# Performance work log

Hardware: AMD Instinct MI355X
Metric: run time of the kernel (lower is better)

Reference implementation:

```python
import jax, jax.numpy as jnp
import numpy as np

B, T, D_MODEL = 1, 4096, 1024
H = 16
SEM_DIM, GEO_DIM, ATTN_DIM = 128, 256, 512
SEM_HD, GEO_HD, V_HD = SEM_DIM // H, GEO_DIM // H, ATTN_DIM // H
ROPE_BASE = 10000.0


def _split_heads(x, hd):
    # (B,T,H*hd) -> (B,H,T,hd)
    b, t, _ = x.shape
    return x.reshape(b, t, H, hd).transpose(0, 2, 1, 3)


def _rope(x, pos_offset, base=ROPE_BASE):
    # x: (B,H,T,rot) with rot == full geo head dim (rotate applies to first rot_dim;
    # here rot_dim == geo_head_dim so the whole vector rotates)
    rot = x.shape[-1]
    inv_freq = 1.0 / (base ** (jnp.arange(0, rot, 2, dtype=jnp.float32) / rot))
    t = jnp.arange(pos_offset, pos_offset + x.shape[2], dtype=jnp.float32)
    freqs = t[:, None] * inv_freq[None, :]            # (T, rot/2)
    cos = jnp.cos(freqs).astype(x.dtype)[None, None]  # (1,1,T,rot/2)
    sin = jnp.sin(freqs).astype(x.dtype)[None, None]
    x1, x2 = x[..., : rot // 2], x[..., rot // 2 :]
    return jnp.concatenate([x1 * cos - x2 * sin, x1 * sin + x2 * cos], axis=-1)


def setup_inputs() -> dict:
    key = jax.random.key(0)
    ks = jax.random.split(key, 8)
    s = lambda fan_in: 1.0 / np.sqrt(fan_in)
    inp = {
        "x": jax.random.normal(ks[0], (B, T, D_MODEL), dtype=jnp.float32),
        "q_sem_w": jax.random.uniform(ks[1], (SEM_DIM, D_MODEL), jnp.float32, -s(D_MODEL), s(D_MODEL)),
        "k_sem_w": jax.random.uniform(ks[2], (SEM_DIM, D_MODEL), jnp.float32, -s(D_MODEL), s(D_MODEL)),
        "q_geo_w": jax.random.uniform(ks[3], (GEO_DIM, D_MODEL), jnp.float32, -s(D_MODEL), s(D_MODEL)),
        "k_geo_w": jax.random.uniform(ks[4], (GEO_DIM, D_MODEL), jnp.float32, -s(D_MODEL), s(D_MODEL)),
        "v_w": jax.random.uniform(ks[5], (ATTN_DIM, D_MODEL), jnp.float32, -s(D_MODEL), s(D_MODEL)),
        "out_w": jax.random.uniform(ks[6], (D_MODEL, ATTN_DIM), jnp.float32, -s(ATTN_DIM), s(ATTN_DIM)),
        "logit_scale": jnp.zeros((H,), dtype=jnp.float32),
        "attn_mask": jnp.tril(jnp.ones((T, T), dtype=bool)),  # causal: True = attend
        "pos_offset": 0,
    }
    return inp


def reference(x, q_sem_w, k_sem_w, q_geo_w, k_geo_w, v_w, out_w, logit_scale, attn_mask, pos_offset):
    dt = x.dtype
    ninf = jnp.finfo(dt).min
    # decoupled projections
    qs = _split_heads(x @ q_sem_w.T, SEM_HD)   # (B,H,T,sem_hd)
    ksem = _split_heads(x @ k_sem_w.T, SEM_HD)
    qg = _split_heads(x @ q_geo_w.T, GEO_HD)   # (B,H,T,geo_hd)
    kg = _split_heads(x @ k_geo_w.T, GEO_HD)
    v = _split_heads(x @ v_w.T, V_HD)          # (B,H,T,v_hd)
    # RoPE on geometric stream only
    qg = _rope(qg, pos_offset)
    kg = _rope(kg, pos_offset)
    # combined scores, scaled as one concatenated QK dot product
    scale = 1.0 / np.sqrt(SEM_HD + GEO_HD)
    scores = (jnp.einsum("bhtd,bhsd->bhts", qs, ksem)
              + jnp.einsum("bhtd,bhsd->bhts", qg, kg)) * scale
    # learned per-head temperature
    scores = scores * jnp.exp(logit_scale)[None, :, None, None]
    scores = jnp.where(attn_mask[None, None], scores, ninf)
    attn = jax.nn.softmax(scores, axis=-1)
    out = jnp.einsum("bhts,bhsd->bhtd", attn, v)       # (B,H,T,v_hd)
    out = out.transpose(0, 2, 1, 3).reshape(B, T, ATTN_DIM)
    return out @ out_w.T                                # (B,T,d_model)
```

## Files before the change

kernel.cpp:

```cpp
#include <hip/hip_runtime.h>
#include <hip/hip_bf16.h>

typedef __attribute__((ext_vector_type(8))) short short8;
typedef __attribute__((ext_vector_type(4))) short short4v;
typedef __attribute__((ext_vector_type(4))) float f32x4;

#define TT 4096
#define DM 1024
#define NH 16
#define NPROJ 1280
#define DATTN 512

static __device__ __forceinline__ short f2bf(float f) {
  __hip_bfloat16 h = __float2bfloat16(f);
  return *reinterpret_cast<short*>(&h);
}
static __device__ __forceinline__ float bf2f(__hip_bfloat16 h) { return __bfloat162float(h); }

__global__ __launch_bounds__(256) void k_f32_to_bf16(const float* __restrict__ in,
                                                     __hip_bfloat16* __restrict__ out, int n4) {
  int i = blockIdx.x * blockDim.x + threadIdx.x;
  if (i >= n4) return;
  float4 v = reinterpret_cast<const float4*>(in)[i];
  short4v o;
  o[0] = f2bf(v.x); o[1] = f2bf(v.y); o[2] = f2bf(v.z); o[3] = f2bf(v.w);
  reinterpret_cast<short4v*>(out)[i] = o;
}

__global__ __launch_bounds__(256) void k_pack_wcat(const float* __restrict__ qs,
    const float* __restrict__ ks, const float* __restrict__ qg, const float* __restrict__ kg,
    const float* __restrict__ vw, __hip_bfloat16* __restrict__ w, int n4) {
  int i = blockIdx.x * blockDim.x + threadIdx.x;
  if (i >= n4) return;
  int idx = i * 4;
  int row = idx >> 10;
  int col = idx & 1023;
  const float* src;
  if (row < 128)      src = qs + (size_t)row * DM;
  else if (row < 256) src = ks + (size_t)(row - 128) * DM;
  else if (row < 512) src = qg + (size_t)(row - 256) * DM;
  else if (row < 768) src = kg + (size_t)(row - 512) * DM;
  else                src = vw + (size_t)(row - 768) * DM;
  float4 v = *reinterpret_cast<const float4*>(src + col);
  short4v o;
  o[0] = f2bf(v.x); o[1] = f2bf(v.y); o[2] = f2bf(v.z); o[3] = f2bf(v.w);
  *reinterpret_cast<short4v*>(w + idx) = o;
}

template<int OUT_BF16>
__global__ __launch_bounds__(256) void k_gemm_bt(const __hip_bfloat16* __restrict__ A,
    const __hip_bfloat16* __restrict__ B, void* __restrict__ Cv, int M, int N, int K) {
  __shared__ alignas(16) __hip_bfloat16 lA[128 * 32];
  __shared__ alignas(16) __hip_bfloat16 lB[128 * 32];
  const int tid = threadIdx.x;
  const int lane = tid & 63;
  const int wid = tid >> 6;
  const int m0 = blockIdx.x * 128, n0 = blockIdx.y * 128;
  const int wm = (wid >> 1) * 64, wn = (wid & 1) * 64;
  const int srow = tid >> 2;
  const int scol = (tid & 3) * 8;
  const int fr = lane & 15, fk = (lane >> 4) * 8;
  f32x4 acc[4][4];
  const f32x4 zz = {0.f, 0.f, 0.f, 0.f};
#pragma unroll
  for (int m = 0; m < 4; ++m)
#pragma unroll
    for (int n = 0; n < 4; ++n) acc[m][n] = zz;

  for (int kt = 0; kt < K; kt += 32) {
    __syncthreads();
    {
      const __hip_bfloat16* ga0 = A + (size_t)(m0 + srow) * K + kt + scol;
      const __hip_bfloat16* ga1 = A + (size_t)(m0 + 64 + srow) * K + kt + scol;
      const __hip_bfloat16* gb0 = B + (size_t)(n0 + srow) * K + kt + scol;
      const __hip_bfloat16* gb1 = B + (size_t)(n0 + 64 + srow) * K + kt + scol;
      __builtin_amdgcn_global_load_lds((const __attribute__((address_space(1))) void*)ga0,
          (__attribute__((address_space(3))) void*)(lA + srow * 32 + scol), 16, 0, 0);
      __builtin_amdgcn_global_load_lds((const __attribute__((address_space(1))) void*)ga1,
          (__attribute__((address_space(3))) void*)(lA + (64 + srow) * 32 + scol), 16, 0, 0);
      __builtin_amdgcn_global_load_lds((const __attribute__((address_space(1))) void*)gb0,
          (__attribute__((address_space(3))) void*)(lB + srow * 32 + scol), 16, 0, 0);
      __builtin_amdgcn_global_load_lds((const __attribute__((address_space(1))) void*)gb1,
          (__attribute__((address_space(3))) void*)(lB + (64 + srow) * 32 + scol), 16, 0, 0);
    }
    __syncthreads();
    short8 af[4], bfr[4];
#pragma unroll
    for (int m = 0; m < 4; ++m)
      af[m] = *reinterpret_cast<const short8*>(lA + (wm + m * 16 + fr) * 32 + fk);
#pragma unroll
    for (int n = 0; n < 4; ++n)
      bfr[n] = *reinterpret_cast<const short8*>(lB + (wn + n * 16 + fr) * 32 + fk);
#pragma unroll
    for (int m = 0; m < 4; ++m)
#pragma unroll
      for (int n = 0; n < 4; ++n)
        acc[m][n] = __builtin_amdgcn_mfma_f32_16x16x32_bf16(af[m], bfr[n], acc[m][n], 0, 0, 0);
  }
  const int cr = (lane >> 4) * 4, cc = lane & 15;
#pragma unroll
  for (int m = 0; m < 4; ++m)
#pragma unroll
    for (int n = 0; n < 4; ++n)
#pragma unroll
      for (int j = 0; j < 4; ++j) {
        const int row = m0 + wm + m * 16 + cr + j;
        const int col = n0 + wn + n * 16 + cc;
        if (OUT_BF16)
          ((__hip_bfloat16*)Cv)[(size_t)row * N + col] = __float2bfloat16(acc[m][n][j]);
        else
          ((float*)Cv)[(size_t)row * N + col] = acc[m][n][j];
      }
}

__global__ __launch_bounds__(256) void k_rope_pack(const __hip_bfloat16* __restrict__ proj,
    const float* __restrict__ ls, const int* __restrict__ posp,
    __hip_bfloat16* __restrict__ Qp, __hip_bfloat16* __restrict__ Kp,
    __hip_bfloat16* __restrict__ Vt) {
  const int gid = blockIdx.x * blockDim.x + threadIdx.x;
  const int t = gid & (TT - 1);
  const int h = gid >> 12;
  const __hip_bfloat16* pr = proj + (size_t)t * NPROJ;
  const float qscale = 0.20412414523193154f * 1.4426950408889634f * __expf(ls[h]);
  const float pos = (float)(t + posp[0]);
  const float invf[8] = {1.0f, 0.31622776601683794f, 0.1f, 0.031622776601683794f,
                         0.01f, 0.0031622776601683794f, 0.001f, 0.00031622776601683794f};
  short8 qv[4], kv[4];
  const short8 z8 = {0, 0, 0, 0, 0, 0, 0, 0};
  qv[3] = z8; kv[3] = z8;
#pragma unroll
  for (int i = 0; i < 8; ++i) {
    qv[0][i] = f2bf(bf2f(pr[h * 8 + i]) * qscale);
    kv[0][i] = f2bf(bf2f(pr[128 + h * 8 + i]));
  }
#pragma unroll
  for (int i = 0; i < 8; ++i) {
    const float ang = pos * invf[i];
    float ss, cc;
    __sincosf(ang, &ss, &cc);
    const float x1q = bf2f(pr[256 + h * 16 + i]), x2q = bf2f(pr[256 + h * 16 + 8 + i]);
    const float x1k = bf2f(pr[512 + h * 16 + i]), x2k = bf2f(pr[512 + h * 16 + 8 + i]);
    qv[1][i] = f2bf((x1q * cc - x2q * ss) * qscale);
    qv[2][i] = f2bf((x1q * ss + x2q * cc) * qscale);
    kv[1][i] = f2bf(x1k * cc - x2k * ss);
    kv[2][i] = f2bf(x1k * ss + x2k * cc);
  }
  short8* qdst = reinterpret_cast<short8*>(Qp + ((size_t)h * TT + t) * 32);
  short8* kdst = reinterpret_cast<short8*>(Kp + ((size_t)h * TT + t) * 32);
#pragma unroll
  for (int p = 0; p < 4; ++p) { qdst[p] = qv[p]; kdst[p] = kv[p]; }
#pragma unroll
  for (int i = 0; i < 32; ++i)
    Vt[((size_t)h * 32 + i) * TT + t] = pr[768 + h * 32 + i];
}

__global__ __launch_bounds__(256) void k_attn(const __hip_bfloat16* __restrict__ Qp,
    const __hip_bfloat16* __restrict__ Kp, const __hip_bfloat16* __restrict__ Vt,
    __hip_bfloat16* __restrict__ Ob) {
  __shared__ alignas(16) __hip_bfloat16 lK[2][64 * 32];
  __shared__ alignas(16) __hip_bfloat16 lV[2][32 * 64];
  __shared__ alignas(16) __hip_bfloat16 Plds[4][16][72];
  const int lin = blockIdx.x;
  const int xcd = lin & 7;
  const int idx = lin >> 3;
  const int h = xcd * 2 + (idx & 1);
  const int qb = 63 - (idx >> 1);
  const int nt = qb + 1;
  const int tid = threadIdx.x;
  const int lane = tid & 63, w = tid >> 6;
  const int g = lane >> 4, c = lane & 15;
  const int krow = (tid >> 6) * 16 + (tid & 15);
  const int kcol = ((tid >> 4) & 3) * 8;
  const int vrow = ((tid >> 6) & 1) * 16 + (tid & 15);
  const int vcol = ((tid >> 7) & 1) * 32 + ((tid >> 4) & 3) * 8;
  const __hip_bfloat16* Kh = Kp + (size_t)h * TT * 32 + (size_t)krow * 32 + kcol;
  const __hip_bfloat16* Vh = Vt + (size_t)h * 32 * TT + (size_t)vrow * TT + vcol;
  const f32x4 zz = {0.f, 0.f, 0.f, 0.f};

  const int qrow = qb * 64 + w * 16 + c;
  const short8 qf =
      *reinterpret_cast<const short8*>(Qp + ((size_t)h * TT + qrow) * 32 + 8 * g);
  f32x4 o0 = zz, o1 = zz;
  float mst = -1e30f, lsum = 0.f;
  int cur = 0;
  __builtin_amdgcn_global_load_lds(
      (const __attribute__((address_space(1))) void*)Kh,
      (__attribute__((address_space(3))) void*)(lK[0] + tid * 8), 16, 0, 0);
  __builtin_amdgcn_global_load_lds(
      (const __attribute__((address_space(1))) void*)Vh,
      (__attribute__((address_space(3))) void*)(lV[0] + tid * 8), 16, 0, 0);

  for (int it = 0; it < nt; ++it) {
    __syncthreads();
    if (it + 1 < nt) {
      const int kv1 = (it + 1) * 64;
      __builtin_amdgcn_global_load_lds(
          (const __attribute__((address_space(1))) void*)(Kh + (size_t)kv1 * 32),
          (__attribute__((address_space(3))) void*)(lK[cur ^ 1] + tid * 8), 16, 0, 0);
      __builtin_amdgcn_global_load_lds(
          (const __attribute__((address_space(1))) void*)(Vh + kv1),
          (__attribute__((address_space(3))) void*)(lV[cur ^ 1] + tid * 8), 16, 0, 0);
    }
    const char* kb = (const char*)lK[cur];
    short8 kf[4];
#pragma unroll
    for (int ct = 0; ct < 4; ++ct)
      kf[ct] = *reinterpret_cast<const short8*>(kb + ct * 1024 + lane * 16);
    const char* vb = (const char*)lV[cur];
    const short8 v00 = *reinterpret_cast<const short8*>(vb + lane * 16);
    const short8 v10 = *reinterpret_cast<const short8*>(vb + 1024 + lane * 16);
    const short8 v01 = *reinterpret_cast<const short8*>(vb + 2048 + lane * 16);
    const short8 v11 = *reinterpret_cast<const short8*>(vb + 3072 + lane * 16);
    f32x4 s[4];
#pragma unroll
    for (int ct = 0; ct < 4; ++ct)
      s[ct] = __builtin_amdgcn_mfma_f32_16x16x32_bf16(kf[ct], qf, zz, 0, 0, 0);
    if (it == nt - 1) {
#pragma unroll
      for (int ct = 0; ct < 4; ++ct)
#pragma unroll
        for (int j = 0; j < 4; ++j)
          if (ct * 16 + g * 4 + j > w * 16 + c) s[ct][j] = -1e30f;
    }
    float m01 = fmaxf(fmaxf(s[0][0], s[0][1]), fmaxf(s[0][2], s[0][3]));
    float m23 = fmaxf(fmaxf(s[1][0], s[1][1]), fmaxf(s[1][2], s[1][3]));
    float m45 = fmaxf(fmaxf(s[2][0], s[2][1]), fmaxf(s[2][2], s[2][3]));
    float m67 = fmaxf(fmaxf(s[3][0], s[3][1]), fmaxf(s[3][2], s[3][3]));
    float pm_ = fmaxf(fmaxf(m01, m23), fmaxf(m45, m67));
    if (__any(pm_ > mst + 8.0f)) {
      float pm2 = fmaxf(pm_, __shfl_xor(pm_, 16, 64));
      pm2 = fmaxf(pm2, __shfl_xor(pm2, 32, 64));
      const float nm = fmaxf(mst, pm2);
      const float alpha = exp2f(mst - nm);
      mst = nm;
      lsum *= alpha;
#pragma unroll
      for (int j = 0; j < 4; ++j) { o0[j] *= alpha; o1[j] *= alpha; }
    }
    float ts = 0.f;
#pragma unroll
    for (int ct = 0; ct < 4; ++ct) {
#pragma unroll
      for (int j = 0; j < 4; ++j) s[ct][j] = exp2f(s[ct][j] - mst);
      ts += (s[ct][0] + s[ct][1]) + (s[ct][2] + s[ct][3]);
    }
    lsum += ts;
#pragma unroll
    for (int ct = 0; ct < 4; ++ct) {
      float2 p01; p01.x = s[ct][0]; p01.y = s[ct][1];
      float2 p23; p23.x = s[ct][2]; p23.y = s[ct][3];
      __hip_bfloat162 b01 = __float22bfloat162_rn(p01);
      __hip_bfloat162 b23 = __float22bfloat162_rn(p23);
      *reinterpret_cast<__hip_bfloat162*>(&Plds[w][c][ct * 16 + g * 4]) = b01;
      *reinterpret_cast<__hip_bfloat162*>(&Plds[w][c][ct * 16 + g * 4 + 2]) = b23;
    }
    const short8 pf0 = *reinterpret_cast<const short8*>(&Plds[w][c][8 * g]);
    const short8 pf1 = *reinterpret_cast<const short8*>(&Plds[w][c][32 + 8 * g]);
    o0 = __builtin_amdgcn_mfma_f32_16x16x32_bf16(v00, pf0, o0, 0, 0, 0);
    o0 = __builtin_amdgcn_mfma_f32_16x16x32_bf16(v01, pf1, o0, 0, 0, 0);
    o1 = __builtin_amdgcn_mfma_f32_16x16x32_bf16(v10, pf0, o1, 0, 0, 0);
    o1 = __builtin_amdgcn_mfma_f32_16x16x32_bf16(v11, pf1, o1, 0, 0, 0);
    cur ^= 1;
  }
  lsum += __shfl_xor(lsum, 16, 64);
  lsum += __shfl_xor(lsum, 32, 64);
  const float inv = 1.0f / lsum;
  __hip_bfloat16* dst = Ob + (size_t)qrow * DATTN + h * 32;
  short4v w0, w1;
#pragma unroll
  for (int j = 0; j < 4; ++j) { w0[j] = f2bf(o0[j] * inv); w1[j] = f2bf(o1[j] * inv); }
  *reinterpret_cast<short4v*>(dst + g * 4) = w0;
  *reinterpret_cast<short4v*>(dst + 16 + g * 4) = w1;
}

extern "C" void kernel_launch(void* const* d_in, const int* in_sizes, int n_in,
                              void* d_out, int out_size, void* d_ws, size_t ws_size,
                              hipStream_t stream) {
  const float* x   = (const float*)d_in[0];
  const float* qsw = (const float*)d_in[1];
  const float* ksw = (const float*)d_in[2];
  const float* qgw = (const float*)d_in[3];
  const float* kgw = (const float*)d_in[4];
  const float* vw  = (const float*)d_in[5];
  const float* ow  = (const float*)d_in[6];
  const float* ls  = (const float*)d_in[7];
  const int* posp  = (const int*)d_in[9];

  size_t off = 0;
  auto alloc = [&](size_t bytes) {
    char* p = (char*)d_ws + off;
    off += (bytes + 255) & ~(size_t)255;
    return (void*)p;
  };
  __hip_bfloat16* Xbf  = (__hip_bfloat16*)alloc((size_t)TT * DM * 2);
  __hip_bfloat16* Wcat = (__hip_bfloat16*)alloc((size_t)NPROJ * DM * 2);
  __hip_bfloat16* OW   = (__hip_bfloat16*)alloc((size_t)DM * DATTN * 2);
  __hip_bfloat16* proj = (__hip_bfloat16*)alloc((size_t)TT * NPROJ * 2);
  __hip_bfloat16* Qp   = (__hip_bfloat16*)alloc((size_t)NH * TT * 32 * 2);
  __hip_bfloat16* Kpk  = (__hip_bfloat16*)alloc((size_t)NH * TT * 32 * 2);
  __hip_bfloat16* Vt   = (__hip_bfloat16*)alloc((size_t)NH * 32 * TT * 2);
  __hip_bfloat16* Ob   = (__hip_bfloat16*)alloc((size_t)TT * DATTN * 2);

  k_f32_to_bf16<<<dim3((TT * DM / 4) / 256), 256, 0, stream>>>(x, Xbf, TT * DM / 4);
  k_f32_to_bf16<<<dim3((DM * DATTN / 4) / 256), 256, 0, stream>>>(ow, OW, DM * DATTN / 4);
  k_pack_wcat<<<dim3((NPROJ * DM / 4) / 256), 256, 0, stream>>>(qsw, ksw, qgw, kgw, vw, Wcat,
                                                                NPROJ * DM / 4);
  k_gemm_bt<1><<<dim3(TT / 128, NPROJ / 128), 256, 0, stream>>>(Xbf, Wcat, (void*)proj,
                                                                TT, NPROJ, DM);
  k_rope_pack<<<dim3(TT * NH / 256), 256, 0, stream>>>(proj, ls, posp, Qp, Kpk, Vt);
  k_attn<<<dim3(1024), 256, 0, stream>>>(Qp, Kpk, Vt, Ob);
  k_gemm_bt<0><<<dim3(TT / 128, DM / 128), 256, 0, stream>>>(Ob, OW, (void*)d_out,
                                                             TT, DM, DATTN);
}
```

Baseline: 131.8 us.

## Triple-buffer K/V tiles with explicit vmcnt waits and fold max shift into MFMA

Moves the attention K/V staging from double to triple buffering, prefetching two tiles ahead and replacing __syncthreads with explicit vmcnt waits plus a raw barrier. The running-max subtraction is folded into the MFMA accumulator input, so the score exponent no longer needs a separate subtract per element. It also adds s_setprio around the MFMA groups and packs the bf16 P stores into one 64-bit write. This is meant to hide global-load latency and trim VALU work, at the cost of more LDS per block, which may reduce occupancy, and of relying on hand-counted vmcnt correctness.

```diff
diff --git a/kernel.cpp b/kernel.cpp
--- a/kernel.cpp
+++ b/kernel.cpp
@@ -16,6 +16,11 @@
   return *reinterpret_cast<short*>(&h);
 }
 static __device__ __forceinline__ float bf2f(__hip_bfloat16 h) { return __bfloat162float(h); }
+static __device__ __forceinline__ unsigned pk2(float a, float b) {
+  float2 t; t.x = a; t.y = b;
+  __hip_bfloat162 r = __float22bfloat162_rn(t);
+  return *reinterpret_cast<unsigned*>(&r);
+}
 
 __global__ __launch_bounds__(256) void k_f32_to_bf16(const float* __restrict__ in,
                                                      __hip_bfloat16* __restrict__ out, int n4) {
@@ -157,8 +162,8 @@
 __global__ __launch_bounds__(256) void k_attn(const __hip_bfloat16* __restrict__ Qp,
     const __hip_bfloat16* __restrict__ Kp, const __hip_bfloat16* __restrict__ Vt,
     __hip_bfloat16* __restrict__ Ob) {
-  __shared__ alignas(16) __hip_bfloat16 lK[2][64 * 32];
-  __shared__ alignas(16) __hip_bfloat16 lV[2][32 * 64];
+  __shared__ alignas(16) __hip_bfloat16 lK[3][64 * 32];
+  __shared__ alignas(16) __hip_bfloat16 lV[3][32 * 64];
   __shared__ alignas(16) __hip_bfloat16 Plds[4][16][72];
   const int lin = blockIdx.x;
   const int xcd = lin & 7;
@@ -181,26 +186,31 @@
   const short8 qf =
       *reinterpret_cast<const short8*>(Qp + ((size_t)h * TT + qrow) * 32 + 8 * g);
   f32x4 o0 = zz, o1 = zz;
-  float mst = -1e30f, lsum = 0.f;
+  float mshift = 0.f;
+  float lsum = 0.f;
+
+  auto stage = [&](int tile, int buf) {
+    const int kv = tile * 64;
+    __builtin_amdgcn_global_load_lds(
+        (const __attribute__((address_space(1))) void*)(Kh + (size_t)kv * 32),
+        (__attribute__((address_space(3))) void*)(lK[buf] + tid * 8), 16, 0, 0);
+    __builtin_amdgcn_global_load_lds(
+        (const __attribute__((address_space(1))) void*)(Vh + kv),
+        (__attribute__((address_space(3))) void*)(lV[buf] + tid * 8), 16, 0, 0);
+  };
+
+  stage(0, 0);
+  if (nt > 1) stage(1, 1);
   int cur = 0;
-  __builtin_amdgcn_global_load_lds(
-      (const __attribute__((address_space(1))) void*)Kh,
-      (__attribute__((address_space(3))) void*)(lK[0] + tid * 8), 16, 0, 0);
-  __builtin_amdgcn_global_load_lds(
-      (const __attribute__((address_space(1))) void*)Vh,
-      (__attribute__((address_space(3))) void*)(lV[0] + tid * 8), 16, 0, 0);
-
   for (int it = 0; it < nt; ++it) {
-    __syncthreads();
     if (it + 1 < nt) {
-      const int kv1 = (it + 1) * 64;
-      __builtin_amdgcn_global_load_lds(
-          (const __attribute__((address_space(1))) void*)(Kh + (size_t)kv1 * 32),
-          (__attribute__((address_space(3))) void*)(lK[cur ^ 1] + tid * 8), 16, 0, 0);
-      __builtin_amdgcn_global_load_lds(
-          (const __attribute__((address_space(1))) void*)(Vh + kv1),
-          (__attribute__((address_space(3))) void*)(lV[cur ^ 1] + tid * 8), 16, 0, 0);
-    }
+      asm volatile("s_waitcnt vmcnt(2)" ::: "memory");
+    } else {
+      asm volatile("s_waitcnt vmcnt(0)" ::: "memory");
+    }
+    __builtin_amdgcn_s_barrier();
+    __builtin_amdgcn_sched_barrier(0);
+    if (it + 2 < nt) stage(it + 2, cur == 0 ? 2 : cur - 1);
     const char* kb = (const char*)lK[cur];
     short8 kf[4];
 #pragma unroll
@@ -211,10 +221,13 @@
     const short8 v10 = *reinterpret_cast<const short8*>(vb + 1024 + lane * 16);
     const short8 v01 = *reinterpret_cast<const short8*>(vb + 2048 + lane * 16);
     const short8 v11 = *reinterpret_cast<const short8*>(vb + 3072 + lane * 16);
+    const f32x4 cin = {-mshift, -mshift, -mshift, -mshift};
     f32x4 s[4];
+    __builtin_amdgcn_s_setprio(1);
 #pragma unroll
     for (int ct = 0; ct < 4; ++ct)
-      s[ct] = __builtin_amdgcn_mfma_f32_16x16x32_bf16(kf[ct], qf, zz, 0, 0, 0);
+      s[ct] = __builtin_amdgcn_mfma_f32_16x16x32_bf16(kf[ct], qf, cin, 0, 0, 0);
+    __builtin_amdgcn_s_setprio(0);
     if (it == nt - 1) {
 #pragma unroll
       for (int ct = 0; ct < 4; ++ct)
@@ -227,40 +240,44 @@
     float m45 = fmaxf(fmaxf(s[2][0], s[2][1]), fmaxf(s[2][2], s[2][3]));
     float m67 = fmaxf(fmaxf(s[3][0], s[3][1]), fmaxf(s[3][2], s[3][3]));
     float pm_ = fmaxf(fmaxf(m01, m23), fmaxf(m45, m67));
-    if (__any(pm_ > mst + 8.0f)) {
+    if (__any(pm_ > 8.0f)) {
       float pm2 = fmaxf(pm_, __shfl_xor(pm_, 16, 64));
       pm2 = fmaxf(pm2, __shfl_xor(pm2, 32, 64));
-      const float nm = fmaxf(mst, pm2);
-      const float alpha = exp2f(mst - nm);
-      mst = nm;
+      const float delta = fmaxf(pm2, 0.f);
+      const float alpha = exp2f(-delta);
+      mshift += delta;
       lsum *= alpha;
 #pragma unroll
       for (int j = 0; j < 4; ++j) { o0[j] *= alpha; o1[j] *= alpha; }
+#pragma unroll
+      for (int ct = 0; ct < 4; ++ct)
+#pragma unroll
+        for (int j = 0; j < 4; ++j) s[ct][j] -= delta;
     }
     float ts = 0.f;
 #pragma unroll
     for (int ct = 0; ct < 4; ++ct) {
 #pragma unroll
-      for (int j = 0; j < 4; ++j) s[ct][j] = exp2f(s[ct][j] - mst);
+      for (int j = 0; j < 4; ++j) s[ct][j] = exp2f(s[ct][j]);
       ts += (s[ct][0] + s[ct][1]) + (s[ct][2] + s[ct][3]);
     }
     lsum += ts;
 #pragma unroll
     for (int ct = 0; ct < 4; ++ct) {
-      float2 p01; p01.x = s[ct][0]; p01.y = s[ct][1];
-      float2 p23; p23.x = s[ct][2]; p23.y = s[ct][3];
-      __hip_bfloat162 b01 = __float22bfloat162_rn(p01);
-      __hip_bfloat162 b23 = __float22bfloat162_rn(p23);
-      *reinterpret_cast<__hip_bfloat162*>(&Plds[w][c][ct * 16 + g * 4]) = b01;
-      *reinterpret_cast<__hip_bfloat162*>(&Plds[w][c][ct * 16 + g * 4 + 2]) = b23;
+      uint2 u;
+      u.x = pk2(s[ct][0], s[ct][1]);
+      u.y = pk2(s[ct][2], s[ct][3]);
+      *reinterpret_cast<uint2*>(&Plds[w][c][ct * 16 + g * 4]) = u;
     }
     const short8 pf0 = *reinterpret_cast<const short8*>(&Plds[w][c][8 * g]);
     const short8 pf1 = *reinterpret_cast<const short8*>(&Plds[w][c][32 + 8 * g]);
+    __builtin_amdgcn_s_setprio(1);
     o0 = __builtin_amdgcn_mfma_f32_16x16x32_bf16(v00, pf0, o0, 0, 0, 0);
     o0 = __builtin_amdgcn_mfma_f32_16x16x32_bf16(v01, pf1, o0, 0, 0, 0);
     o1 = __builtin_amdgcn_mfma_f32_16x16x32_bf16(v10, pf0, o1, 0, 0, 0);
     o1 = __builtin_amdgcn_mfma_f32_16x16x32_bf16(v11, pf1, o1, 0, 0, 0);
-    cur ^= 1;
+    __builtin_amdgcn_s_setprio(0);
+    cur = (cur == 2) ? 0 : cur + 1;
   }
   lsum += __shfl_xor(lsum, 16, 64);
   lsum += __shfl_xor(lsum, 32, 64);
```

New measurement: 135.9 us. 3.1% more time.
